# Optimization experiments

Hardware: AMD Instinct MI355X
Metric: run time of the kernel (lower is better)

## Reference

```python
import jax, jax.numpy as jnp
import numpy as np

B, NUNIT_ALL, NCOL = 128, 1024, 8


def setup_inputs() -> dict:
    key = jax.random.key(0)
    k1, k2, k3 = jax.random.split(key, 3)
    x = jax.random.normal(k1, (B, NUNIT_ALL * NUNIT_ALL), dtype=jnp.float32)
    u = jax.random.normal(k2, (NUNIT_ALL // 2, NCOL), dtype=jnp.float32)
    v = jax.random.normal(k3, (NUNIT_ALL // 2, NCOL), dtype=jnp.float32)
    return {"x": x, "u": u, "v": v}


def reference(x, u, v):
    # u, v: (nUnit, ncol); nUnit_all = 2*nUnit
    nunit, ncol = u.shape
    n_all = 2 * nunit
    # normalize u, v jointly by the column norms of concat([u, v], axis=0)
    uv_norm = jnp.linalg.norm(jnp.concatenate([u, v], axis=0), axis=0, keepdims=True)
    un = u / uv_norm
    vn = v / uv_norm
    z = jnp.zeros_like(un)
    uo = jnp.concatenate([un, z], axis=0)   # (n_all, ncol)
    ov = jnp.concatenate([z, vn], axis=0)   # (n_all, ncol)
    b = x.shape[0]
    x3 = x.reshape(b, n_all, n_all)         # per-sample Jacobian J
    # projections J @ uo, J @ ov : (b, n_all, ncol)
    uo_f = jnp.einsum('bij,jc->bic', x3, uo)
    ov_f = jnp.einsum('bij,jc->bic', x3, ov)
    # quadratic forms per column c: (b, ncol)
    uJu = jnp.einsum('ic,bic->bc', uo, uo_f)
    vJu = jnp.einsum('ic,bic->bc', ov, uo_f)
    uJv = jnp.einsum('ic,bic->bc', uo, ov_f)
    vJv = jnp.einsum('ic,bic->bc', ov, ov_f)
    return jnp.concatenate([uJu, vJu, uJv, vJv], axis=-1)  # (b, 4*ncol)
```

## Files before the change

kernel.cpp:

```cpp
#include <hip/hip_runtime.h>

#define NALL 1024
#define NH   512
#define NCOL 8
#define ROWS_PER_BLOCK 64
#define THREADS 256
#define CHUNKS (NALL / ROWS_PER_BLOCK)
#define SAMPLES 2

typedef float f32x4 __attribute__((ext_vector_type(4)));

__global__ __launch_bounds__(THREADS) void jxy_kernel(
    const float* __restrict__ x, const float* __restrict__ u,
    const float* __restrict__ v, float* __restrict__ out) {
    const int bid   = blockIdx.x;
    const int pair  = bid >> 4;
    const int chunk = bid & (CHUNKS - 1);
    const int r0    = chunk * ROWS_PER_BLOCK;
    const int ih    = (r0 >= NH) ? 1 : 0;
    const int rloc  = r0 - ih * NH;

    const int tid  = threadIdx.x;
    const int wave = tid >> 6;
    const int lane = tid & 63;
    const int jbase = wave * 256 + lane * 4;
    const int jh    = (jbase >= NH) ? 1 : 0;
    const int jloc  = jbase - jh * NH;

    __shared__ float red[THREADS];
    __shared__ float inv_norm[NCOL];
    {
        const int c   = tid & 7;
        const int seg = tid >> 3;
        float s = 0.f;
        for (int r = seg; r < NH; r += 32) {
            float a = u[r * NCOL + c];
            float bb = v[r * NCOL + c];
            s = fmaf(a, a, fmaf(bb, bb, s));
        }
        red[tid] = s;
        __syncthreads();
        for (int off = THREADS / 2; off >= NCOL; off >>= 1) {
            if (tid < off) red[tid] += red[tid + off];
            __syncthreads();
        }
        if (tid < NCOL) inv_norm[tid] = 1.0f / sqrtf(red[tid]);
        __syncthreads();
    }

    __shared__ __align__(16) float wl[ROWS_PER_BLOCK * NCOL];
    const float* rawl = ih ? v : u;
    for (int idx = tid; idx < ROWS_PER_BLOCK * NCOL; idx += THREADS)
        wl[idx] = rawl[rloc * NCOL + idx] * inv_norm[idx & 7];

    const float* rawr = jh ? v : u;
    float wr[4][NCOL];
#pragma unroll
    for (int k = 0; k < 4; ++k) {
        const float4* p = reinterpret_cast<const float4*>(rawr + (size_t)(jloc + k) * NCOL);
        float4 a = p[0];
        float4 bq = p[1];
        wr[k][0] = a.x * inv_norm[0];  wr[k][1] = a.y * inv_norm[1];
        wr[k][2] = a.z * inv_norm[2];  wr[k][3] = a.w * inv_norm[3];
        wr[k][4] = bq.x * inv_norm[4]; wr[k][5] = bq.y * inv_norm[5];
        wr[k][6] = bq.z * inv_norm[6]; wr[k][7] = bq.w * inv_norm[7];
    }
    __syncthreads();

    for (int s = 0; s < SAMPLES; ++s) {
        const int b = pair * SAMPLES + s;

        float acc[NCOL];
#pragma unroll
        for (int c = 0; c < NCOL; ++c) acc[c] = 0.f;

        const float* xrow = x + ((size_t)b * NALL + r0) * NALL + jbase;

#pragma unroll 8
        for (int r = 0; r < ROWS_PER_BLOCK; ++r) {
            f32x4 xv = __builtin_nontemporal_load(
                reinterpret_cast<const f32x4*>(xrow + (size_t)r * NALL));

            float t[NCOL];
#pragma unroll
            for (int c = 0; c < NCOL; ++c)
                t[c] = fmaf(xv.x, wr[0][c],
                       fmaf(xv.y, wr[1][c],
                       fmaf(xv.z, wr[2][c],
                            xv.w * wr[3][c])));

            float4 wa = *reinterpret_cast<const float4*>(&wl[r * NCOL]);
            float4 wb = *reinterpret_cast<const float4*>(&wl[r * NCOL + 4]);
            acc[0] = fmaf(wa.x, t[0], acc[0]);
            acc[1] = fmaf(wa.y, t[1], acc[1]);
            acc[2] = fmaf(wa.z, t[2], acc[2]);
            acc[3] = fmaf(wa.w, t[3], acc[3]);
            acc[4] = fmaf(wb.x, t[4], acc[4]);
            acc[5] = fmaf(wb.y, t[5], acc[5]);
            acc[6] = fmaf(wb.z, t[6], acc[6]);
            acc[7] = fmaf(wb.w, t[7], acc[7]);
        }

#pragma unroll
        for (int c = 0; c < NCOL; ++c) {
#pragma unroll
            for (int off = 32; off >= 1; off >>= 1)
                acc[c] += __shfl_xor(acc[c], off, 64);
        }

        if (lane == 0) {
            const int q = ih + 2 * jh;
            float* o = out + (size_t)b * (4 * NCOL) + q * NCOL;
#pragma unroll
            for (int c = 0; c < NCOL; ++c)
                atomicAdd(o + c, acc[c]);
        }
    }
}

extern "C" void kernel_launch(void* const* d_in, const int* in_sizes, int n_in,
                              void* d_out, int out_size, void* d_ws, size_t ws_size,
                              hipStream_t stream) {
    const float* x = (const float*)d_in[0];
    const float* u = (const float*)d_in[1];
    const float* v = (const float*)d_in[2];
    float* out = (float*)d_out;

    const int b_count = in_sizes[0] / (NALL * NALL);

    (void)hipMemsetAsync(d_out, 0, (size_t)out_size * sizeof(float), stream);

    dim3 grid((b_count / SAMPLES) * CHUNKS);
    jxy_kernel<<<grid, THREADS, 0, stream>>>(x, u, v, out);
}
```

Baseline: 95.65 us.

## Register double-buffer x row loads and compute norms per-wave without block syncs

Issues the first x row loads before the norm computation, then keeps a two-slot register buffer of 4-row groups so loads for later rows are in flight while earlier rows are processed, spanning both samples in one fully unrolled loop. Each wave now computes the column norms itself using shuffles and fills its own copy of the left weights in shared memory, which removes the block-wide __syncthreads reduction. This trades higher register pressure (launch bounds hint of 4 blocks) and a redundant per-wave norm computation for hiding memory latency in a bandwidth-bound stream.

```diff
diff --git a/kernel.cpp b/kernel.cpp
--- a/kernel.cpp
+++ b/kernel.cpp
@@ -5,12 +5,18 @@
 #define NCOL 8
 #define ROWS_PER_BLOCK 64
 #define THREADS 256
-#define CHUNKS (NALL / ROWS_PER_BLOCK)
+#define CHUNKS 16
 #define SAMPLES 2
+#define BR 4
+#define NSLOT (SAMPLES * ROWS_PER_BLOCK / BR)
 
 typedef float f32x4 __attribute__((ext_vector_type(4)));
 
-__global__ __launch_bounds__(THREADS) void jxy_kernel(
+__device__ __forceinline__ f32x4 nt_load(const float* p) {
+    return __builtin_nontemporal_load(reinterpret_cast<const f32x4*>(p));
+}
+
+__global__ __launch_bounds__(THREADS, 4) void jxy_kernel(
     const float* __restrict__ x, const float* __restrict__ u,
     const float* __restrict__ v, float* __restrict__ out) {
     const int bid   = blockIdx.x;
@@ -27,60 +33,80 @@
     const int jh    = (jbase >= NH) ? 1 : 0;
     const int jloc  = jbase - jh * NH;
 
-    __shared__ float red[THREADS];
-    __shared__ float inv_norm[NCOL];
+    const float* xrow0 = x + ((size_t)(pair * SAMPLES) * NALL + r0) * NALL + jbase;
+    const float* xrow1 = xrow0 + (size_t)NALL * NALL;
+
+    f32x4 buf[2][BR];
+
+#pragma unroll
+    for (int k = 0; k < BR; ++k)
+        buf[0][k] = nt_load(xrow0 + (size_t)k * NALL);
+
+    float nrm[NCOL];
+#pragma unroll
+    for (int c = 0; c < NCOL; ++c) nrm[c] = 0.f;
+    for (int r = lane; r < NH; r += 64) {
+        const f32x4* up = reinterpret_cast<const f32x4*>(u + r * NCOL);
+        const f32x4* vp = reinterpret_cast<const f32x4*>(v + r * NCOL);
+        f32x4 a0 = up[0], a1 = up[1], b0 = vp[0], b1 = vp[1];
+        nrm[0] = fmaf(a0.x, a0.x, fmaf(b0.x, b0.x, nrm[0]));
+        nrm[1] = fmaf(a0.y, a0.y, fmaf(b0.y, b0.y, nrm[1]));
+        nrm[2] = fmaf(a0.z, a0.z, fmaf(b0.z, b0.z, nrm[2]));
+        nrm[3] = fmaf(a0.w, a0.w, fmaf(b0.w, b0.w, nrm[3]));
+        nrm[4] = fmaf(a1.x, a1.x, fmaf(b1.x, b1.x, nrm[4]));
+        nrm[5] = fmaf(a1.y, a1.y, fmaf(b1.y, b1.y, nrm[5]));
+        nrm[6] = fmaf(a1.z, a1.z, fmaf(b1.z, b1.z, nrm[6]));
+        nrm[7] = fmaf(a1.w, a1.w, fmaf(b1.w, b1.w, nrm[7]));
+    }
+#pragma unroll
+    for (int c = 0; c < NCOL; ++c) {
+#pragma unroll
+        for (int off = 32; off >= 1; off >>= 1)
+            nrm[c] += __shfl_xor(nrm[c], off, 64);
+    }
+    float inv[NCOL];
+#pragma unroll
+    for (int c = 0; c < NCOL; ++c) inv[c] = 1.0f / sqrtf(nrm[c]);
+
+    __shared__ __align__(16) float wl[4][ROWS_PER_BLOCK * NCOL];
     {
-        const int c   = tid & 7;
-        const int seg = tid >> 3;
-        float s = 0.f;
-        for (int r = seg; r < NH; r += 32) {
-            float a = u[r * NCOL + c];
-            float bb = v[r * NCOL + c];
-            s = fmaf(a, a, fmaf(bb, bb, s));
-        }
-        red[tid] = s;
-        __syncthreads();
-        for (int off = THREADS / 2; off >= NCOL; off >>= 1) {
-            if (tid < off) red[tid] += red[tid + off];
-            __syncthreads();
-        }
-        if (tid < NCOL) inv_norm[tid] = 1.0f / sqrtf(red[tid]);
-        __syncthreads();
+        const float* rawl = ih ? v : u;
+        const f32x4* rp = reinterpret_cast<const f32x4*>(rawl + (size_t)(rloc + lane) * NCOL);
+        f32x4 l0 = rp[0], l1 = rp[1];
+        l0.x *= inv[0]; l0.y *= inv[1]; l0.z *= inv[2]; l0.w *= inv[3];
+        l1.x *= inv[4]; l1.y *= inv[5]; l1.z *= inv[6]; l1.w *= inv[7];
+        f32x4* wp = reinterpret_cast<f32x4*>(&wl[wave][lane * NCOL]);
+        wp[0] = l0; wp[1] = l1;
     }
-
-    __shared__ __align__(16) float wl[ROWS_PER_BLOCK * NCOL];
-    const float* rawl = ih ? v : u;
-    for (int idx = tid; idx < ROWS_PER_BLOCK * NCOL; idx += THREADS)
-        wl[idx] = rawl[rloc * NCOL + idx] * inv_norm[idx & 7];
 
     const float* rawr = jh ? v : u;
     float wr[4][NCOL];
 #pragma unroll
     for (int k = 0; k < 4; ++k) {
-        const float4* p = reinterpret_cast<const float4*>(rawr + (size_t)(jloc + k) * NCOL);
-        float4 a = p[0];
-        float4 bq = p[1];
-        wr[k][0] = a.x * inv_norm[0];  wr[k][1] = a.y * inv_norm[1];
-        wr[k][2] = a.z * inv_norm[2];  wr[k][3] = a.w * inv_norm[3];
-        wr[k][4] = bq.x * inv_norm[4]; wr[k][5] = bq.y * inv_norm[5];
-        wr[k][6] = bq.z * inv_norm[6]; wr[k][7] = bq.w * inv_norm[7];
+        const f32x4* p = reinterpret_cast<const f32x4*>(rawr + (size_t)(jloc + k) * NCOL);
+        f32x4 a = p[0], bq = p[1];
+        wr[k][0] = a.x * inv[0];  wr[k][1] = a.y * inv[1];
+        wr[k][2] = a.z * inv[2];  wr[k][3] = a.w * inv[3];
+        wr[k][4] = bq.x * inv[4]; wr[k][5] = bq.y * inv[5];
+        wr[k][6] = bq.z * inv[6]; wr[k][7] = bq.w * inv[7];
     }
-    __syncthreads();
 
-    for (int s = 0; s < SAMPLES; ++s) {
-        const int b = pair * SAMPLES + s;
+#pragma unroll
+    for (int k = 0; k < BR; ++k)
+        buf[1][k] = nt_load(xrow0 + (size_t)(BR + k) * NALL);
 
-        float acc[NCOL];
+    const float* wlw = &wl[wave][0];
+    const int q = ih + 2 * jh;
+    float acc[NCOL];
 #pragma unroll
-        for (int c = 0; c < NCOL; ++c) acc[c] = 0.f;
+    for (int c = 0; c < NCOL; ++c) acc[c] = 0.f;
 
-        const float* xrow = x + ((size_t)b * NALL + r0) * NALL + jbase;
-
-#pragma unroll 8
-        for (int r = 0; r < ROWS_PER_BLOCK; ++r) {
-            f32x4 xv = __builtin_nontemporal_load(
-                reinterpret_cast<const f32x4*>(xrow + (size_t)r * NALL));
-
+#pragma unroll
+    for (int i = 0; i < NSLOT; ++i) {
+        const int rb = (i & 15) * BR;
+#pragma unroll
+        for (int k = 0; k < BR; ++k) {
+            f32x4 xv = buf[i & 1][k];
             float t[NCOL];
 #pragma unroll
             for (int c = 0; c < NCOL; ++c)
@@ -88,9 +114,9 @@
                        fmaf(xv.y, wr[1][c],
                        fmaf(xv.z, wr[2][c],
                             xv.w * wr[3][c])));
-
-            float4 wa = *reinterpret_cast<const float4*>(&wl[r * NCOL]);
-            float4 wb = *reinterpret_cast<const float4*>(&wl[r * NCOL + 4]);
+            const int row = rb + k;
+            f32x4 wa = *reinterpret_cast<const f32x4*>(&wlw[row * NCOL]);
+            f32x4 wb = *reinterpret_cast<const f32x4*>(&wlw[row * NCOL + 4]);
             acc[0] = fmaf(wa.x, t[0], acc[0]);
             acc[1] = fmaf(wa.y, t[1], acc[1]);
             acc[2] = fmaf(wa.z, t[2], acc[2]);
@@ -100,20 +126,30 @@
             acc[6] = fmaf(wb.z, t[6], acc[6]);
             acc[7] = fmaf(wb.w, t[7], acc[7]);
         }
-
+        if (i + 2 < NSLOT) {
+            const int ns = i + 2;
+            const float* nb = (ns < NSLOT / 2) ? xrow0 : xrow1;
+            const int nrb = (ns & 15) * BR;
 #pragma unroll
-        for (int c = 0; c < NCOL; ++c) {
+            for (int k = 0; k < BR; ++k)
+                buf[i & 1][k] = nt_load(nb + (size_t)(nrb + k) * NALL);
+        }
+        if (i == NSLOT / 2 - 1 || i == NSLOT - 1) {
+            const int s = (i >= NSLOT / 2) ? 1 : 0;
 #pragma unroll
-            for (int off = 32; off >= 1; off >>= 1)
-                acc[c] += __shfl_xor(acc[c], off, 64);
-        }
-
-        if (lane == 0) {
-            const int q = ih + 2 * jh;
-            float* o = out + (size_t)b * (4 * NCOL) + q * NCOL;
+            for (int c = 0; c < NCOL; ++c) {
 #pragma unroll
-            for (int c = 0; c < NCOL; ++c)
-                atomicAdd(o + c, acc[c]);
+                for (int off = 32; off >= 1; off >>= 1)
+                    acc[c] += __shfl_xor(acc[c], off, 64);
+            }
+            if (lane == 0) {
+                float* o = out + (size_t)(pair * SAMPLES + s) * (4 * NCOL) + q * NCOL;
+#pragma unroll
+                for (int c = 0; c < NCOL; ++c)
+                    atomicAdd(o + c, acc[c]);
+            }
+#pragma unroll
+            for (int c = 0; c < NCOL; ++c) acc[c] = 0.f;
         }
     }
 }
```

Result: slower. 98.68 us (+3.2%).
